# Performance work log

Hardware: AMD Instinct MI355X
Metric: run time of the kernel (lower is better)

## Reference

```python
import jax, jax.numpy as jnp
import numpy as np

B, T, I, H = 8192, 2048, 2, 20


def setup_inputs() -> dict:
    key = jax.random.key(0)
    ks = jax.random.split(key, 7)
    s = 1.0 / np.sqrt(H).astype(np.float32)  # PyTorch RNN/Linear init bound
    u = lambda k, shp: jax.random.uniform(k, shp, minval=-s, maxval=s, dtype=jnp.float32)
    return {
        "x": jax.random.normal(ks[0], (B, T, I), dtype=jnp.float32),
        "W_ih": u(ks[1], (H, I)),
        "W_hh": u(ks[2], (H, H)),
        "b_ih": u(ks[3], (H,)),
        "b_hh": u(ks[4], (H,)),
        "fc_w": u(ks[5], (1, H)),
        "fc_b": u(ks[6], (1,)),
    }


def reference(x, W_ih, W_hh, b_ih, b_hh, fc_w, fc_b):
    # x: [B, T, I] (batch_first). Precompute input contribution for all steps.
    # xw: [T, B, H] -- time-major for lax.scan
    xw = jnp.einsum("bti,hi->tbh", x, W_ih) + b_ih + b_hh
    h0 = jnp.zeros((x.shape[0], H), dtype=x.dtype)

    def step(h, xw_t):
        h_new = jnp.tanh(xw_t + h @ W_hh.T)  # tanh-RNN recurrence
        return h_new, None

    hT, _ = jax.lax.scan(step, h0, xw)
    out = hT @ fc_w.T + fc_b          # fc on last timestep: [B, 1]
    h_state = hT[None]                # [1, B, H] like nn.RNN's h_n
    return out, h_state
```

## Files before the change

kernel.cpp:

```cpp
#include <hip/hip_runtime.h>


#define T_STEPS 2048
#define B_ROWS  8192
#define NCHUNK  (T_STEPS / 8)

#define XOR1_CTRL 0xB1
#define XOR2_CTRL 0x4E
#define MIR7_CTRL 0x141

__device__ __forceinline__ float tanh_fast(float a) {
    float e = __builtin_amdgcn_exp2f(a * 2.8853900817779268f);
    float r = __builtin_amdgcn_rcpf(e + 1.0f);
    return fmaf(-2.0f, r, 1.0f);
}

__device__ __forceinline__ float2 fma2(float2 a, float2 b, float2 c) {
    return make_float2(fmaf(a.x, b.x, c.x), fmaf(a.y, b.y, c.y));
}

template <int CTRL>
__device__ __forceinline__ void dpp_to(float& dst, float src) {
    dst = __int_as_float(__builtin_amdgcn_update_dpp(
        __float_as_int(dst), __float_as_int(src), CTRL, 0xF, 0xF, false));
}

template <int CTRL>
__device__ __forceinline__ float dpp_full(float v) {
    return __int_as_float(__builtin_amdgcn_update_dpp(
        0, __float_as_int(v), CTRL, 0xF, 0xF, true));
}

__global__ __launch_bounds__(64, 1) void rnn_fused(
    const float* __restrict__ x,
    const float* __restrict__ W_ih,
    const float* __restrict__ W_hh,
    const float* __restrict__ b_ih,
    const float* __restrict__ b_hh,
    const float* __restrict__ fc_w,
    const float* __restrict__ fc_b,
    float* __restrict__ out)
{
    const int lane = threadIdx.x & 63;
    const int g    = lane & 7;
    const int r    = lane >> 3;
    const int row  = blockIdx.x * 8 + r;

    const int M[8] = {0, 7, 1, 6, 2, 5, 3, 4};

    float2 W2[3][12];
    float  wi0[3], wi1[3], bsum[3], fcw[3];
#pragma unroll
    for (int jj = 0; jj < 3; ++jj) {
        const int j = 3 * g + jj;
        const bool v = (j < 20);
#pragma unroll
        for (int p = 0; p < 12; ++p) {
            float wv[2];
#pragma unroll
            for (int h = 0; h < 2; ++h) {
                const int slot = 2 * p + h;
                const int k = 3 * (g ^ M[slot / 3]) + (slot % 3);
                wv[h] = (v && k < 20) ? W_hh[j * 20 + k] : 0.0f;
            }
            W2[jj][p] = make_float2(wv[0], wv[1]);
        }
        wi0[jj]  = v ? W_ih[j * 2 + 0] : 0.0f;
        wi1[jj]  = v ? W_ih[j * 2 + 1] : 0.0f;
        bsum[jj] = v ? (b_ih[j] + b_hh[j]) : 0.0f;
        fcw[jj]  = v ? fc_w[j] : 0.0f;
    }

    float hg[24];
#pragma unroll
    for (int i = 0; i < 24; ++i) hg[i] = 0.0f;

    auto step = [&](float x0, float x1) {
        float2 c0 = make_float2(fmaf(x0, wi0[0], bsum[0]), x1 * wi1[0]);
        float2 c1 = make_float2(fmaf(x0, wi0[1], bsum[1]), x1 * wi1[1]);
        float2 c2 = make_float2(fmaf(x0, wi0[2], bsum[2]), x1 * wi1[2]);
#pragma unroll
        for (int p = 0; p < 12; ++p) {
            const float2 hp = make_float2(hg[2 * p], hg[2 * p + 1]);
            c0 = fma2(hp, W2[0][p], c0);
            c1 = fma2(hp, W2[1][p], c1);
            c2 = fma2(hp, W2[2][p], c2);
        }
        hg[0] = tanh_fast(c0.x + c0.y);
        hg[1] = tanh_fast(c1.x + c1.y);
        hg[2] = tanh_fast(c2.x + c2.y);
        dpp_to<MIR7_CTRL>(hg[3], hg[0]);
        dpp_to<MIR7_CTRL>(hg[4], hg[1]);
        dpp_to<MIR7_CTRL>(hg[5], hg[2]);
#pragma unroll
        for (int i = 0; i < 6; ++i)  dpp_to<XOR1_CTRL>(hg[6 + i], hg[i]);
#pragma unroll
        for (int i = 0; i < 12; ++i) dpp_to<XOR2_CTRL>(hg[12 + i], hg[i]);
    };

    const float4* xq = (const float4*)(x + (size_t)row * (T_STEPS * 2));
    float4 q[4], qn[4];
#pragma unroll
    for (int i = 0; i < 4; ++i) q[i] = xq[i];

#pragma unroll 1
    for (int c = 0; c < NCHUNK; c += 2) {
        const int c1 = c + 1;
        const int c2 = (c + 2 < NCHUNK) ? (c + 2) : c1;
#pragma unroll
        for (int i = 0; i < 4; ++i) qn[i] = xq[4 * c1 + i];

        step(q[0].x, q[0].y); step(q[0].z, q[0].w);
        step(q[1].x, q[1].y); step(q[1].z, q[1].w);
        step(q[2].x, q[2].y); step(q[2].z, q[2].w);
        step(q[3].x, q[3].y); step(q[3].z, q[3].w);

#pragma unroll
        for (int i = 0; i < 4; ++i) q[i] = xq[4 * c2 + i];

        step(qn[0].x, qn[0].y); step(qn[0].z, qn[0].w);
        step(qn[1].x, qn[1].y); step(qn[1].z, qn[1].w);
        step(qn[2].x, qn[2].y); step(qn[2].z, qn[2].w);
        step(qn[3].x, qn[3].y); step(qn[3].z, qn[3].w);
    }

    {
        const int j0 = 3 * g;
        float* hs = out + B_ROWS + (size_t)row * 20;
        if (j0 + 0 < 20) hs[j0 + 0] = hg[0];
        if (j0 + 1 < 20) hs[j0 + 1] = hg[1];
        if (j0 + 2 < 20) hs[j0 + 2] = hg[2];
    }
    {
        float p = hg[0] * fcw[0];
        p = fmaf(hg[1], fcw[1], p);
        p = fmaf(hg[2], fcw[2], p);
        p += dpp_full<XOR1_CTRL>(p);
        p += dpp_full<XOR2_CTRL>(p);
        p += dpp_full<MIR7_CTRL>(p);
        if (g == 0) out[row] = p + fc_b[0];
    }
}

extern "C" void kernel_launch(void* const* d_in, const int* in_sizes, int n_in,
                              void* d_out, int out_size, void* d_ws, size_t ws_size,
                              hipStream_t stream) {
    const float* x    = (const float*)d_in[0];
    const float* W_ih = (const float*)d_in[1];
    const float* W_hh = (const float*)d_in[2];
    const float* b_ih = (const float*)d_in[3];
    const float* b_hh = (const float*)d_in[4];
    const float* fc_w = (const float*)d_in[5];
    const float* fc_b = (const float*)d_in[6];
    float* out = (float*)d_out;

    rnn_fused<<<1024, 64, 0, stream>>>(x, W_ih, W_hh, b_ih, b_hh, fc_w, fc_b, out);
}
```

Baseline: 569.8 us.

## Interleave two batch rows per lane to increase instruction-level parallelism

Each wave now processes two independent batch rows in an interleaved recurrence, so the FMA, tanh and DPP chains of one row can overlap with those of the other. The grid is halved accordingly and the x prefetch is resized to two float4 per row per chunk. This targets the latency-bound serial dependency chain of the recurrence, at the cost of doubled register use and fewer waves across the GPU, which may leave SIMDs idle.

```diff
diff --git a/kernel.cpp b/kernel.cpp
--- a/kernel.cpp
+++ b/kernel.cpp
@@ -3,7 +3,7 @@
 
 #define T_STEPS 2048
 #define B_ROWS  8192
-#define NCHUNK  (T_STEPS / 8)
+#define NCHUNK  (T_STEPS / 4)
 
 #define XOR1_CTRL 0xB1
 #define XOR2_CTRL 0x4E
@@ -44,7 +44,8 @@
     const int lane = threadIdx.x & 63;
     const int g    = lane & 7;
     const int r    = lane >> 3;
-    const int row  = blockIdx.x * 8 + r;
+    const int rowA = blockIdx.x * 16 + r;
+    const int rowB = rowA + 8;
 
     const int M[8] = {0, 7, 1, 6, 2, 5, 3, 4};
 
@@ -71,74 +72,110 @@
         fcw[jj]  = v ? fc_w[j] : 0.0f;
     }
 
-    float hg[24];
+    float hgA[24], hgB[24];
 #pragma unroll
-    for (int i = 0; i < 24; ++i) hg[i] = 0.0f;
+    for (int i = 0; i < 24; ++i) { hgA[i] = 0.0f; hgB[i] = 0.0f; }
 
-    auto step = [&](float x0, float x1) {
-        float2 c0 = make_float2(fmaf(x0, wi0[0], bsum[0]), x1 * wi1[0]);
-        float2 c1 = make_float2(fmaf(x0, wi0[1], bsum[1]), x1 * wi1[1]);
-        float2 c2 = make_float2(fmaf(x0, wi0[2], bsum[2]), x1 * wi1[2]);
+    auto step = [&](float a0, float a1, float b0, float b1) {
+        float2 cA0 = make_float2(fmaf(a0, wi0[0], bsum[0]), a1 * wi1[0]);
+        float2 cA1 = make_float2(fmaf(a0, wi0[1], bsum[1]), a1 * wi1[1]);
+        float2 cA2 = make_float2(fmaf(a0, wi0[2], bsum[2]), a1 * wi1[2]);
+        float2 cB0 = make_float2(fmaf(b0, wi0[0], bsum[0]), b1 * wi1[0]);
+        float2 cB1 = make_float2(fmaf(b0, wi0[1], bsum[1]), b1 * wi1[1]);
+        float2 cB2 = make_float2(fmaf(b0, wi0[2], bsum[2]), b1 * wi1[2]);
 #pragma unroll
         for (int p = 0; p < 12; ++p) {
-            const float2 hp = make_float2(hg[2 * p], hg[2 * p + 1]);
-            c0 = fma2(hp, W2[0][p], c0);
-            c1 = fma2(hp, W2[1][p], c1);
-            c2 = fma2(hp, W2[2][p], c2);
+            const float2 hpA = make_float2(hgA[2 * p], hgA[2 * p + 1]);
+            const float2 hpB = make_float2(hgB[2 * p], hgB[2 * p + 1]);
+            cA0 = fma2(hpA, W2[0][p], cA0);
+            cB0 = fma2(hpB, W2[0][p], cB0);
+            cA1 = fma2(hpA, W2[1][p], cA1);
+            cB1 = fma2(hpB, W2[1][p], cB1);
+            cA2 = fma2(hpA, W2[2][p], cA2);
+            cB2 = fma2(hpB, W2[2][p], cB2);
         }
-        hg[0] = tanh_fast(c0.x + c0.y);
-        hg[1] = tanh_fast(c1.x + c1.y);
-        hg[2] = tanh_fast(c2.x + c2.y);
-        dpp_to<MIR7_CTRL>(hg[3], hg[0]);
-        dpp_to<MIR7_CTRL>(hg[4], hg[1]);
-        dpp_to<MIR7_CTRL>(hg[5], hg[2]);
+        hgA[0] = tanh_fast(cA0.x + cA0.y);
+        hgB[0] = tanh_fast(cB0.x + cB0.y);
+        hgA[1] = tanh_fast(cA1.x + cA1.y);
+        hgB[1] = tanh_fast(cB1.x + cB1.y);
+        hgA[2] = tanh_fast(cA2.x + cA2.y);
+        hgB[2] = tanh_fast(cB2.x + cB2.y);
+        dpp_to<MIR7_CTRL>(hgA[3], hgA[0]);
+        dpp_to<MIR7_CTRL>(hgB[3], hgB[0]);
+        dpp_to<MIR7_CTRL>(hgA[4], hgA[1]);
+        dpp_to<MIR7_CTRL>(hgB[4], hgB[1]);
+        dpp_to<MIR7_CTRL>(hgA[5], hgA[2]);
+        dpp_to<MIR7_CTRL>(hgB[5], hgB[2]);
 #pragma unroll
-        for (int i = 0; i < 6; ++i)  dpp_to<XOR1_CTRL>(hg[6 + i], hg[i]);
+        for (int i = 0; i < 6; ++i) {
+            dpp_to<XOR1_CTRL>(hgA[6 + i], hgA[i]);
+            dpp_to<XOR1_CTRL>(hgB[6 + i], hgB[i]);
+        }
 #pragma unroll
-        for (int i = 0; i < 12; ++i) dpp_to<XOR2_CTRL>(hg[12 + i], hg[i]);
+        for (int i = 0; i < 12; ++i) {
+            dpp_to<XOR2_CTRL>(hgA[12 + i], hgA[i]);
+            dpp_to<XOR2_CTRL>(hgB[12 + i], hgB[i]);
+        }
     };
 
-    const float4* xq = (const float4*)(x + (size_t)row * (T_STEPS * 2));
-    float4 q[4], qn[4];
+    const float4* xqA = (const float4*)(x + (size_t)rowA * (T_STEPS * 2));
+    const float4* xqB = (const float4*)(x + (size_t)rowB * (T_STEPS * 2));
+    float4 qA[2], qnA[2], qB[2], qnB[2];
 #pragma unroll
-    for (int i = 0; i < 4; ++i) q[i] = xq[i];
+    for (int i = 0; i < 2; ++i) { qA[i] = xqA[i]; qB[i] = xqB[i]; }
 
 #pragma unroll 1
     for (int c = 0; c < NCHUNK; c += 2) {
         const int c1 = c + 1;
         const int c2 = (c + 2 < NCHUNK) ? (c + 2) : c1;
 #pragma unroll
-        for (int i = 0; i < 4; ++i) qn[i] = xq[4 * c1 + i];
+        for (int i = 0; i < 2; ++i) {
+            qnA[i] = xqA[2 * c1 + i];
+            qnB[i] = xqB[2 * c1 + i];
+        }
 
-        step(q[0].x, q[0].y); step(q[0].z, q[0].w);
-        step(q[1].x, q[1].y); step(q[1].z, q[1].w);
-        step(q[2].x, q[2].y); step(q[2].z, q[2].w);
-        step(q[3].x, q[3].y); step(q[3].z, q[3].w);
+        step(qA[0].x, qA[0].y, qB[0].x, qB[0].y);
+        step(qA[0].z, qA[0].w, qB[0].z, qB[0].w);
+        step(qA[1].x, qA[1].y, qB[1].x, qB[1].y);
+        step(qA[1].z, qA[1].w, qB[1].z, qB[1].w);
 
 #pragma unroll
-        for (int i = 0; i < 4; ++i) q[i] = xq[4 * c2 + i];
+        for (int i = 0; i < 2; ++i) {
+            qA[i] = xqA[2 * c2 + i];
+            qB[i] = xqB[2 * c2 + i];
+        }
 
-        step(qn[0].x, qn[0].y); step(qn[0].z, qn[0].w);
-        step(qn[1].x, qn[1].y); step(qn[1].z, qn[1].w);
-        step(qn[2].x, qn[2].y); step(qn[2].z, qn[2].w);
-        step(qn[3].x, qn[3].y); step(qn[3].z, qn[3].w);
+        step(qnA[0].x, qnA[0].y, qnB[0].x, qnB[0].y);
+        step(qnA[0].z, qnA[0].w, qnB[0].z, qnB[0].w);
+        step(qnA[1].x, qnA[1].y, qnB[1].x, qnB[1].y);
+        step(qnA[1].z, qnA[1].w, qnB[1].z, qnB[1].w);
     }
 
     {
         const int j0 = 3 * g;
-        float* hs = out + B_ROWS + (size_t)row * 20;
-        if (j0 + 0 < 20) hs[j0 + 0] = hg[0];
-        if (j0 + 1 < 20) hs[j0 + 1] = hg[1];
-        if (j0 + 2 < 20) hs[j0 + 2] = hg[2];
+        float* hsA = out + B_ROWS + (size_t)rowA * 20;
+        float* hsB = out + B_ROWS + (size_t)rowB * 20;
+        if (j0 + 0 < 20) { hsA[j0 + 0] = hgA[0]; hsB[j0 + 0] = hgB[0]; }
+        if (j0 + 1 < 20) { hsA[j0 + 1] = hgA[1]; hsB[j0 + 1] = hgB[1]; }
+        if (j0 + 2 < 20) { hsA[j0 + 2] = hgA[2]; hsB[j0 + 2] = hgB[2]; }
     }
     {
-        float p = hg[0] * fcw[0];
-        p = fmaf(hg[1], fcw[1], p);
-        p = fmaf(hg[2], fcw[2], p);
-        p += dpp_full<XOR1_CTRL>(p);
-        p += dpp_full<XOR2_CTRL>(p);
-        p += dpp_full<MIR7_CTRL>(p);
-        if (g == 0) out[row] = p + fc_b[0];
+        float pA = hgA[0] * fcw[0];
+        pA = fmaf(hgA[1], fcw[1], pA);
+        pA = fmaf(hgA[2], fcw[2], pA);
+        float pB = hgB[0] * fcw[0];
+        pB = fmaf(hgB[1], fcw[1], pB);
+        pB = fmaf(hgB[2], fcw[2], pB);
+        pA += dpp_full<XOR1_CTRL>(pA);
+        pB += dpp_full<XOR1_CTRL>(pB);
+        pA += dpp_full<XOR2_CTRL>(pA);
+        pB += dpp_full<XOR2_CTRL>(pB);
+        pA += dpp_full<MIR7_CTRL>(pA);
+        pB += dpp_full<MIR7_CTRL>(pB);
+        if (g == 0) {
+            out[rowA] = pA + fc_b[0];
+            out[rowB] = pB + fc_b[0];
+        }
     }
 }
 
@@ -154,5 +191,5 @@
     const float* fc_b = (const float*)d_in[6];
     float* out = (float*)d_out;
 
-    rnn_fused<<<1024, 64, 0, stream>>>(x, W_ih, W_hh, b_ih, b_hh, fc_w, fc_b, out);
+    rnn_fused<<<512, 64, 0, stream>>>(x, W_ih, W_hh, b_ih, b_hh, fc_w, fc_b, out);
 }
```

After: 927.2 us. 1.63x slower.
